# Performance work log

Hardware: AMD Instinct MI355X
Metric: run time of the kernel (lower is better)

The kernel has to match this reference:

```python
import jax, jax.numpy as jnp
import numpy as np

B, E, I, H, O = 8192, 8, 512, 1024, 512


def setup_inputs() -> dict:
    key = jax.random.key(0)
    ks = jax.random.split(key, 8)
    # Xavier-uniform-ish scales for expert weights
    s1 = float(np.sqrt(6.0 / (I + H)))
    s2 = float(np.sqrt(6.0 / (H + H)))
    s3 = float(np.sqrt(6.0 / (H + O)))
    return {
        "X": jax.random.normal(ks[0], (B, I), dtype=jnp.float32),
        "W": jax.random.uniform(ks[1], (B, E), dtype=jnp.float32),
        "W1": jax.random.uniform(ks[2], (E, H, I), minval=-s1, maxval=s1, dtype=jnp.float32),
        "b1": jnp.zeros((E, H), dtype=jnp.float32),
        "W2": jax.random.uniform(ks[3], (E, H, H), minval=-s2, maxval=s2, dtype=jnp.float32),
        "b2": jnp.zeros((E, H), dtype=jnp.float32),
        "W3": jax.random.uniform(ks[4], (E, O, H), minval=-s3, maxval=s3, dtype=jnp.float32),
        "b3": jnp.zeros((E, O), dtype=jnp.float32),
    }


def reference(X, W, W1, b1, W2, b2, W3, b3):
    # NOTE: original torch code calls F.softmax(W, dim=1) but discards the
    # result; raw W is used as the per-expert mixing weight. We match that.
    # Layer 1: per-expert linear [B,E,H], then gate-weighted sum over E.
    pre1 = jnp.einsum('bi,ehi->beh', X, W1) + b1          # [B,E,H]
    mid1 = jax.nn.elu(jnp.einsum('be,beh->bh', W, pre1))  # [B,H]
    pre2 = jnp.einsum('bh,egh->beg', mid1, W2) + b2       # [B,E,H]
    mid2 = jax.nn.elu(jnp.einsum('be,beh->bh', W, pre2))  # [B,H]
    pre3 = jnp.einsum('bh,eoh->beo', mid2, W3) + b3       # [B,E,O]
    out = jnp.einsum('be,beo->bo', W, pre3)               # [B,O]
    return out
```

## Files before the change

### kernel.cpp

```cpp
#include <hip/hip_runtime.h>
#include <hip/hip_bf16.h>
#include <cstdint>
#include <cstddef>

typedef __attribute__((ext_vector_type(8))) short bf16x8;
typedef __attribute__((ext_vector_type(8))) unsigned short u16x8;
typedef __attribute__((ext_vector_type(4))) float f32x4;
typedef unsigned short u16;

__device__ __forceinline__ u16 f2bf(float f) {
    unsigned int u = __float_as_uint(f);
    u += 0x7fffu + ((u >> 16) & 1u);
    return (u16)(u >> 16);
}
__device__ __forceinline__ float bf2f(u16 u) {
    return __uint_as_float(((unsigned int)u) << 16);
}

__device__ __forceinline__ void gload16(const void* g, void* l) {
    __builtin_amdgcn_global_load_lds((const __attribute__((address_space(1))) void*)g,
                                     (__attribute__((address_space(3))) void*)l,
                                     16, 0, 0);
}

__global__ void cvt_f32_bf16(const float* __restrict__ in, u16* __restrict__ out, int n4) {
    int i = blockIdx.x * blockDim.x + threadIdx.x;
    if (i < n4) {
        float4 v = ((const float4*)in)[i];
        ushort4 o;
        o.x = f2bf(v.x); o.y = f2bf(v.y); o.z = f2bf(v.z); o.w = f2bf(v.w);
        ((ushort4*)out)[i] = o;
    }
}

__global__ void make_atilde_f32(const float* __restrict__ A, const float* __restrict__ gate,
                                u16* __restrict__ out, int log2K) {
    const size_t idx = ((size_t)blockIdx.x * 256 + threadIdx.x) * 8;
    const int K = 1 << log2K;
    const size_t b = idx >> (log2K + 3);
    const int rem = (int)(idx - (b << (log2K + 3)));
    const int e = rem >> log2K;
    const int k = rem & (K - 1);
    const float g = gate[b * 8 + e];
    const float* src = A + b * (size_t)K + k;
    float4 v0 = ((const float4*)src)[0];
    float4 v1 = ((const float4*)src)[1];
    u16x8 r;
    r[0] = f2bf(g * v0.x); r[1] = f2bf(g * v0.y); r[2] = f2bf(g * v0.z); r[3] = f2bf(g * v0.w);
    r[4] = f2bf(g * v1.x); r[5] = f2bf(g * v1.y); r[6] = f2bf(g * v1.z); r[7] = f2bf(g * v1.w);
    *(u16x8*)(out + idx) = r;
}

__global__ void make_atilde_bf16(const u16* __restrict__ A, const float* __restrict__ gate,
                                 u16* __restrict__ out, int log2K) {
    const size_t idx = ((size_t)blockIdx.x * 256 + threadIdx.x) * 8;
    const int K = 1 << log2K;
    const size_t b = idx >> (log2K + 3);
    const int rem = (int)(idx - (b << (log2K + 3)));
    const int e = rem >> log2K;
    const int k = rem & (K - 1);
    const float g = gate[b * 8 + e];
    u16x8 a = *(const u16x8*)(A + b * (size_t)K + k);
    u16x8 r;
    #pragma unroll
    for (int j = 0; j < 8; ++j) r[j] = f2bf(g * bf2f(a[j]));
    *(u16x8*)(out + idx) = r;
}

__global__ __launch_bounds__(512, 2)
void moe_gemm_2b(const u16* __restrict__ At, const u16* __restrict__ Bw,
                 float* __restrict__ P,
                 int N, int K, int Ktot, int log2nk, int kts, int bxbits) {
    __shared__ char lds[2][65536];

    const int tid  = threadIdx.x;
    const int lane = tid & 63;
    const int wave = tid >> 6;
    const int wm   = wave >> 2;
    const int wn   = wave & 3;
    const int fr   = lane & 15;
    const int fg   = lane >> 4;
    const int swz  = (fr & 7) << 4;

    const int bid  = blockIdx.x;
    const int wgid = (bid & 7) * 32 + (bid >> 3);
    const int bx   = wgid & ((1 << bxbits) - 1);
    const int by   = (wgid >> bxbits) & 31;
    const int s    = wgid >> (bxbits + 5);
    const int m0   = by * 256;
    const int n0   = bx * 256;

    int rowA[2], rowB[2], ldso[2];
    #pragma unroll
    for (int it = 0; it < 2; ++it) {
        const int o  = (it * 8 + wave) * 1024 + lane * 16;
        const int r  = o >> 7;
        const int cb = (o & 127) ^ ((r & 7) << 4);
        rowA[it] = r * (Ktot * 2) + cb;
        rowB[it] = r * (K * 2) + cb;
        ldso[it] = o;
    }

    const char* Ab0 = (const char*)(At + (size_t)m0 * Ktot);
    const char* Ab1 = Ab0 + (size_t)128 * Ktot * 2;
    const char* Bb0 = (const char*)(Bw + (size_t)n0 * K);
    const char* Bb1 = Bb0 + (size_t)128 * K * 2;
    const size_t Best = (size_t)N * K * 2;
    const int nkm = (1 << log2nk) - 1;
    const int kt0 = s * kts;

#define STAGE_A(BUF, KTG) do { \
    const char* _a0 = Ab0 + (size_t)(KTG) * 128; \
    const char* _a1 = Ab1 + (size_t)(KTG) * 128; \
    char* _l = lds[BUF]; \
    gload16(_a0 + rowA[0], _l + ldso[0]); \
    gload16(_a0 + rowA[1], _l + ldso[1]); \
    gload16(_a1 + rowA[0], _l + 16384 + ldso[0]); \
    gload16(_a1 + rowA[1], _l + 16384 + ldso[1]); \
} while (0)

#define STAGE_B(BUF, KTG) do { \
    const int _kg = (KTG); \
    const size_t _bo = (size_t)(_kg >> log2nk) * Best + (size_t)(_kg & nkm) * 128; \
    char* _l = lds[BUF] + 32768; \
    gload16(Bb0 + _bo + rowB[0], _l + ldso[0]); \
    gload16(Bb0 + _bo + rowB[1], _l + ldso[1]); \
    gload16(Bb1 + _bo + rowB[0], _l + 16384 + ldso[0]); \
    gload16(Bb1 + _bo + rowB[1], _l + 16384 + ldso[1]); \
} while (0)

    f32x4 acc[8][4];
    #pragma unroll
    for (int i = 0; i < 8; ++i)
        #pragma unroll
        for (int j = 0; j < 4; ++j) acc[i][j] = f32x4{0.f, 0.f, 0.f, 0.f};

    bf16x8 af[2][4], bfA[2][2], bfB[2][2];

    STAGE_A(0, kt0);
    STAGE_B(0, kt0);
    STAGE_A(1, kt0 + 1);
    __builtin_amdgcn_sched_barrier(0);
    asm volatile("s_waitcnt vmcnt(4)" ::: "memory");
    __builtin_amdgcn_s_barrier();
    __builtin_amdgcn_sched_barrier(0);

    for (int t = 0; t < kts; ++t) {
        const int BUF = t & 1;
        const char* _abase = lds[BUF] + wm * 16384 + fr * 128;
        const char* _bbase = lds[BUF] + 32768 + (wn >> 1) * 16384 + ((wn & 1) * 64 + fr) * 128;
        const int k0 = (fg * 16) ^ swz;
        const int k1 = (64 + fg * 16) ^ swz;

        if (t + 1 < kts) STAGE_B(BUF ^ 1, kt0 + t + 1);

        #pragma unroll
        for (int i = 0; i < 4; ++i) {
            af[0][i] = *(const bf16x8*)(_abase + i * 2048 + k0);
            af[1][i] = *(const bf16x8*)(_abase + i * 2048 + k1);
        }
        #pragma unroll
        for (int j = 0; j < 2; ++j) {
            bfA[0][j] = *(const bf16x8*)(_bbase + j * 2048 + k0);
            bfA[1][j] = *(const bf16x8*)(_bbase + j * 2048 + k1);
        }
        __builtin_amdgcn_s_setprio(1);
        #pragma unroll
        for (int i = 0; i < 4; ++i)
            #pragma unroll
            for (int j = 0; j < 2; ++j) {
                acc[i][j] = __builtin_amdgcn_mfma_f32_16x16x32_bf16(af[0][i], bfA[0][j], acc[i][j], 0, 0, 0);
                acc[i][j] = __builtin_amdgcn_mfma_f32_16x16x32_bf16(af[1][i], bfA[1][j], acc[i][j], 0, 0, 0);
            }
        __builtin_amdgcn_s_setprio(0);

        #pragma unroll
        for (int j = 0; j < 2; ++j) {
            bfB[0][j] = *(const bf16x8*)(_bbase + (2 + j) * 2048 + k0);
            bfB[1][j] = *(const bf16x8*)(_bbase + (2 + j) * 2048 + k1);
        }
        __builtin_amdgcn_s_setprio(1);
        #pragma unroll
        for (int i = 0; i < 4; ++i)
            #pragma unroll
            for (int j = 0; j < 2; ++j) {
                acc[i][2 + j] = __builtin_amdgcn_mfma_f32_16x16x32_bf16(af[0][i], bfB[0][j], acc[i][2 + j], 0, 0, 0);
                acc[i][2 + j] = __builtin_amdgcn_mfma_f32_16x16x32_bf16(af[1][i], bfB[1][j], acc[i][2 + j], 0, 0, 0);
            }
        __builtin_amdgcn_s_setprio(0);

        #pragma unroll
        for (int i = 0; i < 4; ++i) {
            af[0][i] = *(const bf16x8*)(_abase + (4 + i) * 2048 + k0);
            af[1][i] = *(const bf16x8*)(_abase + (4 + i) * 2048 + k1);
        }
        __builtin_amdgcn_s_setprio(1);
        #pragma unroll
        for (int i = 0; i < 4; ++i)
            #pragma unroll
            for (int j = 0; j < 2; ++j) {
                acc[4 + i][2 + j] = __builtin_amdgcn_mfma_f32_16x16x32_bf16(af[0][i], bfB[0][j], acc[4 + i][2 + j], 0, 0, 0);
                acc[4 + i][2 + j] = __builtin_amdgcn_mfma_f32_16x16x32_bf16(af[1][i], bfB[1][j], acc[4 + i][2 + j], 0, 0, 0);
            }
        __builtin_amdgcn_s_setprio(0);

        __builtin_amdgcn_sched_barrier(0);
        __builtin_amdgcn_s_barrier();
        __builtin_amdgcn_sched_barrier(0);

        if (t + 2 < kts) STAGE_A(BUF, kt0 + t + 2);

        __builtin_amdgcn_s_setprio(1);
        #pragma unroll
        for (int i = 0; i < 4; ++i)
            #pragma unroll
            for (int j = 0; j < 2; ++j) {
                acc[4 + i][j] = __builtin_amdgcn_mfma_f32_16x16x32_bf16(af[0][i], bfA[0][j], acc[4 + i][j], 0, 0, 0);
                acc[4 + i][j] = __builtin_amdgcn_mfma_f32_16x16x32_bf16(af[1][i], bfA[1][j], acc[4 + i][j], 0, 0, 0);
            }
        __builtin_amdgcn_s_setprio(0);

        __builtin_amdgcn_sched_barrier(0);
        if (t + 2 < kts) {
            asm volatile("s_waitcnt vmcnt(4)" ::: "memory");
        } else {
            asm volatile("s_waitcnt vmcnt(0)" ::: "memory");
        }
        __builtin_amdgcn_s_barrier();
        __builtin_amdgcn_sched_barrier(0);
    }

    float* Pb = P + ((size_t)s * 8192 + m0 + wm * 128) * N + (n0 + wn * 64);
    #pragma unroll
    for (int mi = 0; mi < 8; ++mi)
        #pragma unroll
        for (int j = 0; j < 4; ++j) {
            const int r = mi * 16 + fg * 4 + j;
            #pragma unroll
            for (int ni = 0; ni < 4; ++ni)
                Pb[(size_t)r * N + ni * 16 + fr] = acc[mi][ni][j];
        }
#undef STAGE_A
#undef STAGE_B
}

template<int S, bool ELU_ACT, bool OUT_BF16>
__global__ void moe_reduce(const float* __restrict__ P,
                           const float* __restrict__ gate,
                           const float* __restrict__ bias,
                           void* __restrict__ outp,
                           int log2N, int n4total) {
    const int stride = gridDim.x * blockDim.x;
    const size_t MN = ((size_t)n4total) * 4;
    for (int i = blockIdx.x * blockDim.x + threadIdx.x; i < n4total; i += stride) {
        const size_t el = (size_t)i * 4;
        const size_t b = el >> log2N;
        const int n = (int)(el & ((1 << log2N) - 1));
        float4 v = ((const float4*)P)[i];
        #pragma unroll
        for (int s = 1; s < S; ++s) {
            float4 p = *(const float4*)(P + (size_t)s * MN + el);
            v.x += p.x; v.y += p.y; v.z += p.z; v.w += p.w;
        }
        #pragma unroll
        for (int e = 0; e < 8; ++e) {
            const float g = gate[b * 8 + e];
            float4 bb = *(const float4*)(bias + ((size_t)e << log2N) + n);
            v.x += g * bb.x; v.y += g * bb.y; v.z += g * bb.z; v.w += g * bb.w;
        }
        if (ELU_ACT) {
            v.x = v.x > 0.f ? v.x : expm1f(v.x);
            v.y = v.y > 0.f ? v.y : expm1f(v.y);
            v.z = v.z > 0.f ? v.z : expm1f(v.z);
            v.w = v.w > 0.f ? v.w : expm1f(v.w);
        }
        if (OUT_BF16) {
            ushort4 o; o.x = f2bf(v.x); o.y = f2bf(v.y); o.z = f2bf(v.z); o.w = f2bf(v.w);
            ((ushort4*)outp)[i] = o;
        } else {
            ((float4*)outp)[i] = v;
        }
    }
}

__global__ void reduce_atilde2(const float* __restrict__ P,
                               const float* __restrict__ gate,
                               const float* __restrict__ bias,
                               u16* __restrict__ At) {
    const int idx = blockIdx.x * 256 + threadIdx.x;
    const int h = (idx & 127) * 8;
    const size_t b = idx >> 7;
    const size_t MH = (size_t)8192 * 1024;
    const float* p = P + b * 1024 + h;
    float4 v0 = ((const float4*)p)[0];
    float4 v1 = ((const float4*)p)[1];
    {
        const float* p1 = p + MH;
        float4 a0 = ((const float4*)p1)[0], a1 = ((const float4*)p1)[1];
        v0.x += a0.x; v0.y += a0.y; v0.z += a0.z; v0.w += a0.w;
        v1.x += a1.x; v1.y += a1.y; v1.z += a1.z; v1.w += a1.w;
    }
    float4 g0 = *(const float4*)&gate[b * 8];
    float4 g1 = *(const float4*)&gate[b * 8 + 4];
    float gg[8] = {g0.x, g0.y, g0.z, g0.w, g1.x, g1.y, g1.z, g1.w};
    #pragma unroll
    for (int e = 0; e < 8; ++e) {
        const float* bb = bias + e * 1024 + h;
        float4 b0 = ((const float4*)bb)[0], b1 = ((const float4*)bb)[1];
        v0.x += gg[e] * b0.x; v0.y += gg[e] * b0.y; v0.z += gg[e] * b0.z; v0.w += gg[e] * b0.w;
        v1.x += gg[e] * b1.x; v1.y += gg[e] * b1.y; v1.z += gg[e] * b1.z; v1.w += gg[e] * b1.w;
    }
    float m[8] = {v0.x, v0.y, v0.z, v0.w, v1.x, v1.y, v1.z, v1.w};
    #pragma unroll
    for (int j = 0; j < 8; ++j) m[j] = m[j] > 0.f ? m[j] : expm1f(m[j]);
    u16* o = At + b * 8192 + h;
    #pragma unroll
    for (int e = 0; e < 8; ++e) {
        u16x8 r;
        #pragma unroll
        for (int j = 0; j < 8; ++j) r[j] = f2bf(gg[e] * m[j]);
        *(u16x8*)(o + e * 1024) = r;
    }
}

extern "C" void kernel_launch(void* const* d_in, const int* in_sizes, int n_in,
                              void* d_out, int out_size, void* d_ws, size_t ws_size,
                              hipStream_t stream) {
    const float* X  = (const float*)d_in[0];
    const float* W  = (const float*)d_in[1];
    const float* W1 = (const float*)d_in[2];
    const float* b1 = (const float*)d_in[3];
    const float* W2 = (const float*)d_in[4];
    const float* b2 = (const float*)d_in[5];
    const float* W3 = (const float*)d_in[6];
    const float* b3 = (const float*)d_in[7];
    float* out = (float*)d_out;

    char* ws = (char*)d_ws;
    u16* W1b  = (u16*)ws;  ws += (size_t)8 * 1024 * 512 * 2;
    u16* W2b  = (u16*)ws;  ws += (size_t)8 * 1024 * 1024 * 2;
    u16* W3b  = (u16*)ws;  ws += (size_t)8 * 512 * 1024 * 2;
    u16* mid1 = (u16*)ws;  ws += (size_t)8192 * 1024 * 2;
    u16* mid2 = (u16*)ws;  ws += (size_t)8192 * 1024 * 2;
    u16* At1  = (u16*)ws;  ws += (size_t)8192 * 4096 * 2;
    u16* At2  = (u16*)ws;  ws += (size_t)8192 * 8192 * 2;
    (void)mid2;

    float* P1 = (float*)At2;
    float* P2 = (float*)At1;
    float* P3 = (float*)At1;

    cvt_f32_bf16<<<4096, 256, 0, stream>>>(W1, W1b, 4194304 / 4);
    cvt_f32_bf16<<<8192, 256, 0, stream>>>(W2, W2b, 8388608 / 4);
    cvt_f32_bf16<<<4096, 256, 0, stream>>>(W3, W3b, 4194304 / 4);

    dim3 blk(256);

    make_atilde_f32<<<16384, blk, 0, stream>>>(X, W, At1, 9);
    moe_gemm_2b<<<256, 512, 0, stream>>>(At1, W1b, P1, 1024, 512, 4096, 3, 32, 2);
    moe_reduce<2, true, true><<<2048, blk, 0, stream>>>(P1, W, b1, (void*)mid1, 10, 8192 * 1024 / 4);

    make_atilde_bf16<<<32768, blk, 0, stream>>>(mid1, W, At2, 10);
    moe_gemm_2b<<<256, 512, 0, stream>>>(At2, W2b, P2, 1024, 1024, 8192, 4, 64, 2);
    reduce_atilde2<<<4096, blk, 0, stream>>>(P2, W, b2, At2);

    moe_gemm_2b<<<256, 512, 0, stream>>>(At2, W3b, P3, 512, 1024, 8192, 4, 32, 1);
    moe_reduce<4, false, false><<<2048, blk, 0, stream>>>(P3, W, b3, (void*)out, 9, 8192 * 512 / 4);
}
```

Measured before the change: 378.4 us.

## Fuse layer-1 GEMM with gated reduce, ELU and layer-2 A-tilde construction

```diff
diff --git a/kernel.cpp b/kernel.cpp
--- a/kernel.cpp
+++ b/kernel.cpp
@@ -51,20 +51,125 @@
     *(u16x8*)(out + idx) = r;
 }
 
-__global__ void make_atilde_bf16(const u16* __restrict__ A, const float* __restrict__ gate,
-                                 u16* __restrict__ out, int log2K) {
-    const size_t idx = ((size_t)blockIdx.x * 256 + threadIdx.x) * 8;
-    const int K = 1 << log2K;
-    const size_t b = idx >> (log2K + 3);
-    const int rem = (int)(idx - (b << (log2K + 3)));
-    const int e = rem >> log2K;
-    const int k = rem & (K - 1);
-    const float g = gate[b * 8 + e];
-    u16x8 a = *(const u16x8*)(A + b * (size_t)K + k);
-    u16x8 r;
-    #pragma unroll
-    for (int j = 0; j < 8; ++j) r[j] = f2bf(g * bf2f(a[j]));
-    *(u16x8*)(out + idx) = r;
+__global__ __launch_bounds__(256, 4)
+void moe_gemm_l1f(const u16* __restrict__ At,
+                  const u16* __restrict__ Bw,
+                  const float* __restrict__ gate,
+                  const float* __restrict__ bias,
+                  u16* __restrict__ At2out,
+                  int N, int K, int Ktot, int log2nk, int kts) {
+    constexpr int BM = 128, BN = 128, BK = 64;
+    __shared__ u16 As[BM * BK];
+    __shared__ u16 Bs[BN * BK];
+
+    const int tid  = threadIdx.x;
+    const int lane = tid & 63;
+    const int wave = tid >> 6;
+    const int wr = wave >> 1, wc = wave & 1;
+    const int fr = lane & 15;
+    const int fg = lane >> 4;
+
+    const int bid = blockIdx.x;
+    const int xcd = bid & 7, idx = bid >> 3;
+    const int bx  = idx & 7;
+    const int by  = xcd * 8 + (idx >> 3);
+    const int m0  = by * BM;
+    const int n0  = bx * BN;
+
+    int rowoffA[4], rowoffB[4], ldsoff[4];
+    #pragma unroll
+    for (int it = 0; it < 4; ++it) {
+        const int c   = it * 4 + wave;
+        const int L   = c * 1024 + lane * 16;
+        const int row = L >> 7;
+        const int cb  = (L & 127) ^ ((row & 7) << 4);
+        rowoffA[it] = row * (Ktot * 2) + cb;
+        rowoffB[it] = row * (K * 2) + cb;
+        ldsoff[it]  = c * 1024;
+    }
+
+    const char* Abase = (const char*)(At + (size_t)m0 * Ktot);
+    const char* Bbase = (const char*)(Bw + (size_t)n0 * K);
+    const size_t Bestride = (size_t)N * K * 2;
+    const int swz    = (fr & 7) << 4;
+    const int nkmask = (1 << log2nk) - 1;
+
+    f32x4 acc[4][4];
+    #pragma unroll
+    for (int a = 0; a < 4; ++a)
+        #pragma unroll
+        for (int b = 0; b < 4; ++b) acc[a][b] = f32x4{0.f, 0.f, 0.f, 0.f};
+
+    for (int kt = 0; kt < kts; ++kt) {
+        __syncthreads();
+        const char* Ab = Abase + kt * 128;
+        const char* Bb = Bbase + (size_t)(kt >> log2nk) * Bestride + (kt & nkmask) * 128;
+        #pragma unroll
+        for (int it = 0; it < 4; ++it) {
+            gload16(Ab + rowoffA[it], (char*)As + ldsoff[it]);
+            gload16(Bb + rowoffB[it], (char*)Bs + ldsoff[it]);
+        }
+        __syncthreads();
+
+        #pragma unroll
+        for (int kk = 0; kk < 2; ++kk) {
+            const int kb = kk * 64 + fg * 16;
+            bf16x8 af[4], bfr[4];
+            #pragma unroll
+            for (int mi = 0; mi < 4; ++mi) {
+                const int r  = wr * 64 + mi * 16 + fr;
+                af[mi]  = *(const bf16x8*)((const char*)As + r * 128 + (kb ^ swz));
+                const int cc = wc * 64 + mi * 16 + fr;
+                bfr[mi] = *(const bf16x8*)((const char*)Bs + cc * 128 + (kb ^ swz));
+            }
+            #pragma unroll
+            for (int mi = 0; mi < 4; ++mi)
+                #pragma unroll
+                for (int ni = 0; ni < 4; ++ni)
+                    acc[mi][ni] = __builtin_amdgcn_mfma_f32_16x16x32_bf16(
+                        af[mi], bfr[ni], acc[mi][ni], 0, 0, 0);
+        }
+    }
+
+    __syncthreads();
+    float* WsL   = (float*)As;
+    float* BiasL = (float*)Bs;
+    {
+        const int j = tid * 4;
+        *(float4*)&WsL[j]   = *(const float4*)&gate[(size_t)(m0 + (j >> 3)) * 8 + (j & 7)];
+        *(float4*)&BiasL[j] = *(const float4*)&bias[(size_t)(j >> 7) * N + n0 + (j & 127)];
+    }
+    __syncthreads();
+
+    float bias8[4][8];
+    #pragma unroll
+    for (int ni = 0; ni < 4; ++ni)
+        #pragma unroll
+        for (int e = 0; e < 8; ++e)
+            bias8[ni][e] = BiasL[e * BN + wc * 64 + ni * 16 + fr];
+
+    #pragma unroll
+    for (int mi = 0; mi < 4; ++mi) {
+        #pragma unroll
+        for (int j = 0; j < 4; ++j) {
+            const int r = wr * 64 + mi * 16 + fg * 4 + j;
+            float g8[8];
+            #pragma unroll
+            for (int e = 0; e < 8; ++e) g8[e] = WsL[r * 8 + e];
+            #pragma unroll
+            for (int ni = 0; ni < 4; ++ni) {
+                float v = acc[mi][ni][j];
+                #pragma unroll
+                for (int e = 0; e < 8; ++e) v += g8[e] * bias8[ni][e];
+                v = v > 0.f ? v : expm1f(v);
+                const int cl = wc * 64 + ni * 16 + fr;
+                const size_t base = (size_t)(m0 + r) * 8192 + n0 + cl;
+                #pragma unroll
+                for (int e = 0; e < 8; ++e)
+                    At2out[base + e * 1024] = f2bf(g8[e] * v);
+            }
+        }
+    }
 }
 
 __global__ __launch_bounds__(512, 2)
@@ -340,13 +445,9 @@
     u16* W1b  = (u16*)ws;  ws += (size_t)8 * 1024 * 512 * 2;
     u16* W2b  = (u16*)ws;  ws += (size_t)8 * 1024 * 1024 * 2;
     u16* W3b  = (u16*)ws;  ws += (size_t)8 * 512 * 1024 * 2;
-    u16* mid1 = (u16*)ws;  ws += (size_t)8192 * 1024 * 2;
-    u16* mid2 = (u16*)ws;  ws += (size_t)8192 * 1024 * 2;
     u16* At1  = (u16*)ws;  ws += (size_t)8192 * 4096 * 2;
     u16* At2  = (u16*)ws;  ws += (size_t)8192 * 8192 * 2;
-    (void)mid2;
-
-    float* P1 = (float*)At2;
+
     float* P2 = (float*)At1;
     float* P3 = (float*)At1;
 
@@ -357,10 +458,8 @@
     dim3 blk(256);
 
     make_atilde_f32<<<16384, blk, 0, stream>>>(X, W, At1, 9);
-    moe_gemm_2b<<<256, 512, 0, stream>>>(At1, W1b, P1, 1024, 512, 4096, 3, 32, 2);
-    moe_reduce<2, true, true><<<2048, blk, 0, stream>>>(P1, W, b1, (void*)mid1, 10, 8192 * 1024 / 4);
-
-    make_atilde_bf16<<<32768, blk, 0, stream>>>(mid1, W, At2, 10);
+    moe_gemm_l1f<<<512, blk, 0, stream>>>(At1, W1b, W, b1, At2, 1024, 512, 4096, 3, 64);
+
     moe_gemm_2b<<<256, 512, 0, stream>>>(At2, W2b, P2, 1024, 1024, 8192, 4, 64, 2);
     reduce_atilde2<<<4096, blk, 0, stream>>>(P2, W, b2, At2);
 
```

Result: faster. 354.3 us (-6.4%).
